# Performance work log

Hardware: AMD Instinct MI355X
Metric: run time of the kernel (lower is better)

## Reference

```python
import jax, jax.numpy as jnp
import numpy as np

B, S, H = 2, 2048, 2048
NH, NKV, HD = 16, 4, 128
NEG = -1e9


def rotate_half(x):
    x1, x2 = x[..., : x.shape[-1] // 2], x[..., x.shape[-1] // 2 :]
    return jnp.concatenate((-x2, x1), axis=-1)


def setup_inputs() -> dict:
    key = jax.random.key(0)
    ks = jax.random.split(key, 6)
    hidden_states = jax.random.normal(ks[0], (B, S, H), dtype=jnp.float32)
    # causal additive mask [B, 1, S, S]
    causal = jnp.tril(jnp.ones((S, S), dtype=bool))
    attention_mask = jnp.where(causal, 0.0, NEG).astype(jnp.float32)
    attention_mask = jnp.broadcast_to(attention_mask, (B, 1, S, S))
    # rotary embeddings, base 10000
    inv_freq = 1.0 / (10000.0 ** (np.arange(0, HD, 2, dtype=np.float32) / HD))
    pos = np.arange(S, dtype=np.float32)
    freqs = np.outer(pos, inv_freq)  # [S, HD/2]
    emb = np.concatenate([freqs, freqs], axis=-1)  # [S, HD]
    cos = jnp.broadcast_to(jnp.asarray(np.cos(emb)), (B, S, HD))
    sin = jnp.broadcast_to(jnp.asarray(np.sin(emb)), (B, S, HD))
    sc = 0.02
    Wq = jax.random.normal(ks[1], (H, NH * HD), dtype=jnp.float32) * sc
    Wk = jax.random.normal(ks[2], (H, NKV * HD), dtype=jnp.float32) * sc
    Wv = jax.random.normal(ks[3], (H, NKV * HD), dtype=jnp.float32) * sc
    Wo = jax.random.normal(ks[4], (H, H), dtype=jnp.float32) * sc
    return {"hidden_states": hidden_states, "attention_mask": attention_mask,
            "cos": cos, "sin": sin, "Wq": Wq, "Wk": Wk, "Wv": Wv, "Wo": Wo}


def reference(hidden_states, attention_mask, cos, sin, Wq, Wk, Wv, Wo):
    b, s, _ = hidden_states.shape
    # projections -> [b, heads, s, hd]
    q = (hidden_states @ Wq).reshape(b, s, NH, HD).transpose(0, 2, 1, 3)
    k = (hidden_states @ Wk).reshape(b, s, NKV, HD).transpose(0, 2, 1, 3)
    v = (hidden_states @ Wv).reshape(b, s, NKV, HD).transpose(0, 2, 1, 3)
    # RoPE (cos/sin unsqueezed at dim 1)
    c, sn = cos[:, None], sin[:, None]
    q = q * c + rotate_half(q) * sn
    k = k * c + rotate_half(k) * sn
    # GQA repeat_kv: [b, nkv, s, hd] -> [b, nh, s, hd]
    n_rep = NH // NKV
    k = jnp.repeat(k, n_rep, axis=1)
    v = jnp.repeat(v, n_rep, axis=1)
    scores = jnp.einsum("bhqd,bhkd->bhqk", q, k) / jnp.sqrt(jnp.float32(HD))
    scores = scores + attention_mask
    probs = jax.nn.softmax(scores.astype(jnp.float32), axis=-1).astype(q.dtype)
    out = jnp.einsum("bhqk,bhkd->bhqd", probs, v)
    out = out.transpose(0, 2, 1, 3).reshape(b, s, NH * HD)
    return out @ Wo
```

## Files before the change

### kernel.cpp

```cpp
#include <hip/hip_runtime.h>
#include <hip/hip_bf16.h>

typedef __bf16 bf16;
typedef __bf16 bf16x4 __attribute__((ext_vector_type(4)));
typedef __bf16 bf16x8 __attribute__((ext_vector_type(8)));
typedef float f32x4 __attribute__((ext_vector_type(4)));

__device__ __forceinline__ void gload_lds16(const void* g, void* l) {
  __builtin_amdgcn_global_load_lds((__attribute__((address_space(1))) void*)(g),
                                   (__attribute__((address_space(3))) void*)(l), 16, 0, 0);
}
__device__ __forceinline__ float fexp2(float x) {
  float r;
  asm volatile("v_exp_f32 %0, %1" : "=v"(r) : "v"(x));
  return r;
}
#define S_WAITCNT_VM(n) asm volatile("s_waitcnt vmcnt(" #n ")" ::: "memory")

__global__ void k_diag(float* __restrict__ o, float v) { o[threadIdx.x] = v; }

__global__ void k_cvt_bf16(const float* __restrict__ x, bf16* __restrict__ y, int n4) {
  int i = blockIdx.x * blockDim.x + threadIdx.x;
  if (i < n4) {
    float4 v = reinterpret_cast<const float4*>(x)[i];
    bf16x4 o = {(bf16)v.x, (bf16)v.y, (bf16)v.z, (bf16)v.w};
    reinterpret_cast<bf16x4*>(y)[i] = o;
  }
}

__global__ void k_transpose_w(const float* __restrict__ W, bf16* __restrict__ Wt, int K, int N) {
  __shared__ float tile[32][33];
  int kb = blockIdx.x * 32, nb = blockIdx.y * 32;
  int tx = threadIdx.x & 31, ty = threadIdx.x >> 5;
#pragma unroll
  for (int i = 0; i < 32; i += 8)
    tile[ty + i][tx] = W[(size_t)(kb + ty + i) * N + nb + tx];
  __syncthreads();
#pragma unroll
  for (int i = 0; i < 32; i += 8)
    Wt[(size_t)(nb + ty + i) * K + kb + tx] = (bf16)tile[tx][ty + i];
}

__global__ void k_transpose_v(const bf16* __restrict__ Cq, bf16* __restrict__ Vt) {
  __shared__ bf16 tile[32][34];
  constexpr int S = 2048, CSTR = 3072;
  int sb = blockIdx.x * 32, db = blockIdx.y * 32, bh = blockIdx.z;
  int b = bh >> 2, kvh = bh & 3;
  int tx = threadIdx.x & 31, ty = threadIdx.x >> 5;
  const bf16* src = Cq + (size_t)b * S * CSTR + 2560 + kvh * 128;
#pragma unroll
  for (int i = 0; i < 32; i += 8)
    tile[ty + i][tx] = src[(size_t)(sb + ty + i) * CSTR + db + tx];
  __syncthreads();
  bf16* dst = Vt + (size_t)bh * 128 * S;
#pragma unroll
  for (int i = 0; i < 32; i += 8)
    dst[(size_t)(db + ty + i) * S + sb + tx] = tile[tx][ty + i];
}

template <typename OT>
__global__ __launch_bounds__(512) void k_gemm3(const bf16* __restrict__ A,
                                               const bf16* __restrict__ B0,
                                               const bf16* __restrict__ B1, int nsplit,
                                               OT* __restrict__ C, int Ncols, int Kd) {
  __shared__ __align__(16) bf16 lds_[65536];
  char* lds = (char*)lds_;
  const int t = threadIdx.x, w = t >> 6, l = t & 63;
  const int lr = l & 15, lk = l >> 4;
  const int gx = gridDim.x, nwg = gx * gridDim.y;
  const int flat = blockIdx.y * gx + blockIdx.x;
  const int vid = (flat & 7) * (nwg >> 3) + (flat >> 3);
  const int m0 = (vid % gx) * 256, n0 = (vid / gx) * 256;
  const int wm = w >> 2, wn = w & 3;
  const bf16* Bt = (n0 < nsplit) ? B0 + (size_t)n0 * Kd : B1 + (size_t)(n0 - nsplit) * Kd;
  const int nkt = Kd >> 6;
  const int srow = l >> 2;
  const int lch = (l & 3) ^ ((srow + (srow >> 2)) & 3);
  auto stA = [&](int tile, int unit) {
    if (tile >= nkt) return;
    const bf16* s = A + (size_t)(m0 + unit * 64 + (w >> 1) * 16 + srow) * Kd +
                    (tile << 6) + (w & 1) * 32 + lch * 8;
    gload_lds16(s, lds + (tile & 1) * 32768 + unit * 8192 + w * 1024);
  };
  auto stB = [&](int tile, int grp) {
    if (tile >= nkt) return;
    const bf16* s = Bt + (size_t)((w >> 1) * 64 + grp * 16 + srow) * Kd +
                    (tile << 6) + (w & 1) * 32 + lch * 8;
    gload_lds16(s, lds + 65536 + (tile & 1) * 32768 + grp * 8192 + w * 1024);
  };
  const int rdoff = lr * 64 + ((lk ^ ((lr + (lr >> 2)) & 3)) << 4);

  f32x4 acc[8][4] = {};
  stA(0, 0); stA(0, 1); stA(0, 2); stA(0, 3);
  stB(0, 0);
  stA(1, 0); stB(0, 1); stA(1, 1); stB(0, 2); stA(1, 2); stB(0, 3);

  for (int kt = 0; kt < nkt; ++kt) {
    const int buf = kt & 1;
    const char* Ab = lds + buf * 32768;
    const char* Bb = lds + 65536 + buf * 32768;
    bf16x8 af[8][2];
#pragma unroll
    for (int p = 0; p < 4; ++p) {
      if (kt + 1 < nkt) { S_WAITCNT_VM(6); } else { S_WAITCNT_VM(0); }
      __builtin_amdgcn_sched_barrier(0);
      __builtin_amdgcn_s_barrier();
      __builtin_amdgcn_sched_barrier(0);
      if (p == 0) stA(kt + 1, 3); else stA(kt + 2, p - 1);
      stB(kt + 1, p);
      if (p == 0) {
#pragma unroll
        for (int i = 0; i < 8; ++i) {
          const char* ub = Ab + (wm * 2 + (i >> 2)) * 8192 + (i & 3) * 2048;
          af[i][0] = *reinterpret_cast<const bf16x8*>(ub + rdoff);
          af[i][1] = *reinterpret_cast<const bf16x8*>(ub + 1024 + rdoff);
        }
      }
      bf16x8 b0 = *reinterpret_cast<const bf16x8*>(Bb + p * 8192 + wn * 2048 + rdoff);
      bf16x8 b1 = *reinterpret_cast<const bf16x8*>(Bb + p * 8192 + wn * 2048 + 1024 + rdoff);
      __builtin_amdgcn_s_setprio(1);
#pragma unroll
      for (int i = 0; i < 8; ++i) {
        acc[i][p] = __builtin_amdgcn_mfma_f32_16x16x32_bf16(af[i][0], b0, acc[i][p], 0, 0, 0);
        acc[i][p] = __builtin_amdgcn_mfma_f32_16x16x32_bf16(af[i][1], b1, acc[i][p], 0, 0, 0);
      }
      __builtin_amdgcn_s_setprio(0);
      __builtin_amdgcn_sched_barrier(0);
    }
  }
#pragma unroll
  for (int i = 0; i < 8; ++i)
#pragma unroll
    for (int j = 0; j < 4; ++j)
#pragma unroll
      for (int r = 0; r < 4; ++r) {
        int row = m0 + wm * 128 + i * 16 + lk * 4 + r;
        int col = n0 + wn * 64 + j * 16 + lr;
        if constexpr (sizeof(OT) == 4)
          C[(size_t)row * Ncols + col] = acc[i][j][r];
        else
          C[(size_t)row * Ncols + col] = (bf16)acc[i][j][r];
      }
}

__global__ void k_rope(bf16* __restrict__ X, const float* __restrict__ cs, const float* __restrict__ sn,
                       int nh, int rowstride, float scale, int total) {
  int idx = blockIdx.x * blockDim.x + threadIdx.x;
  if (idx >= total) return;
  int d = idx & 63;
  int th = idx >> 6;
  int h = th % nh;
  int tok = th / nh;
  size_t base = (size_t)tok * rowstride + h * 128;
  float c = cs[tok * 128 + d], s = sn[tok * 128 + d];
  float x1 = (float)X[base + d];
  float x2 = (float)X[base + d + 64];
  X[base + d] = (bf16)((x1 * c - x2 * s) * scale);
  X[base + d + 64] = (bf16)((x2 * c + x1 * s) * scale);
}

__global__ __launch_bounds__(256) void k_attn(const bf16* __restrict__ Q, const bf16* __restrict__ KV,
                                              const bf16* __restrict__ Vt, bf16* __restrict__ O) {
  constexpr int S = 2048, HD = 128, QSTR = 3072, OSTR = 2048;
  __shared__ __align__(16) bf16 sK[2][64 * 128];
  __shared__ __align__(16) bf16 sV[2][128 * 64];
  __shared__ __align__(16) bf16 sP[4][16][72];
  const int bid = blockIdx.x;
  const int vid = (bid & 7) * 64 + (bid >> 3);
  const int p = vid & 15, bh = vid >> 4;
  const int h = bh & 15, b = bh >> 4;
  const int t = threadIdx.x, w = t >> 6, l = t & 63;
  const int lr = l & 15, lk = l >> 4;
  const int kvh = h >> 2;
  const int swz = (lr & 7) << 4;

  const char* kbase = (const char*)(KV + (size_t)b * S * QSTR + kvh * HD);
  const int krow_l = w * 16 + (l >> 4);
  const int kcol_l = (l & 15) << 4;
  const char* vtbase = (const char*)(Vt + (size_t)(b * 4 + kvh) * HD * S);
  const int vrow_l = w * 32 + (l >> 3);
  const int vcol_l = (l & 7) << 4;
  char* sKb = (char*)sK;
  char* sVb = (char*)sV;
  auto stage = [&](int kvb, int buf) {
#pragma unroll
    for (int c = 0; c < 4; ++c) {
      const int krow = krow_l + c * 4;
      gload_lds16(kbase + (size_t)(kvb + krow) * (QSTR * 2) + (kcol_l ^ ((krow & 7) << 4)),
                  sKb + buf * 16384 + (w * 4 + c) * 1024);
      const int vrow = vrow_l + c * 8;
      gload_lds16(vtbase + (size_t)vrow * (S * 2) + kvb * 2 + (vcol_l ^ ((vrow & 7) << 4)),
                  sVb + buf * 16384 + (w * 4 + c) * 1024);
    }
  };

  for (int seg = 0; seg < 2; ++seg) {
    const int qtl = seg ? (31 - p) : p;
    const int qw = qtl * 64 + w * 16;
    const int ntiles = qtl + 1;
    int cur = 0;
    stage(0, 0);
    const bf16* Qp = Q + (size_t)(b * S + qw + lr) * QSTR + h * HD + lk * 8;
    bf16x8 qf[4];
#pragma unroll
    for (int i = 0; i < 4; ++i) qf[i] = *reinterpret_cast<const bf16x8*>(Qp + i * 32);
    f32x4 oacc[8] = {};
    float mrow[4] = {-3e38f, -3e38f, -3e38f, -3e38f};
    float lsum[4] = {0.f, 0.f, 0.f, 0.f};
    __syncthreads();
    for (int tt = 0; tt < ntiles; ++tt) {
      const int kvb = tt * 64;
      if (tt + 1 < ntiles) stage(kvb + 64, cur ^ 1);
      const char* sKc = sKb + cur * 16384;
      const char* sVc = sVb + cur * 16384;
      float pm[4][4];
#pragma unroll
      for (int c = 0; c < 4; ++c) {
        f32x4 s4 = {};
#pragma unroll
        for (int kf = 0; kf < 4; ++kf) {
          bf16x8 kf8 = *reinterpret_cast<const bf16x8*>(
              sKc + (c * 16 + lr) * 256 + (((kf * 64) + (lk << 4)) ^ swz));
          s4 = __builtin_amdgcn_mfma_f32_16x16x32_bf16(qf[kf], kf8, s4, 0, 0, 0);
        }
#pragma unroll
        for (int r = 0; r < 4; ++r) pm[c][r] = s4[r];
      }
      if (tt == ntiles - 1) {
#pragma unroll
        for (int c = 0; c < 4; ++c) {
          const int col = kvb + c * 16 + lr;
#pragma unroll
          for (int r = 0; r < 4; ++r)
            if (col > qw + lk * 4 + r) pm[c][r] = -3e38f;
        }
      }
      float pmax[4];
#pragma unroll
      for (int r = 0; r < 4; ++r)
        pmax[r] = fmaxf(fmaxf(pm[0][r], pm[1][r]), fmaxf(pm[2][r], pm[3][r]));
      bool hi = (pmax[0] > mrow[0] + 8.f) | (pmax[1] > mrow[1] + 8.f) |
                (pmax[2] > mrow[2] + 8.f) | (pmax[3] > mrow[3] + 8.f);
      if (__any(hi)) {
        float mx[4];
#pragma unroll
        for (int r = 0; r < 4; ++r) mx[r] = pmax[r];
#pragma unroll
        for (int off = 1; off < 16; off <<= 1)
#pragma unroll
          for (int r = 0; r < 4; ++r) mx[r] = fmaxf(mx[r], __shfl_xor(mx[r], off));
#pragma unroll
        for (int r = 0; r < 4; ++r) {
          float mn = fmaxf(mrow[r], mx[r]);
          float fac = fexp2(mrow[r] - mn);
          mrow[r] = mn;
          lsum[r] *= fac;
#pragma unroll
          for (int ch = 0; ch < 8; ++ch) oacc[ch][r] *= fac;
        }
      }
#pragma unroll
      for (int c = 0; c < 4; ++c)
#pragma unroll
        for (int r = 0; r < 4; ++r) pm[c][r] = fexp2(pm[c][r] - mrow[r]);
#pragma unroll
      for (int r = 0; r < 4; ++r)
        lsum[r] += (pm[0][r] + pm[1][r]) + (pm[2][r] + pm[3][r]);
#pragma unroll
      for (int c = 0; c < 4; ++c)
#pragma unroll
        for (int r = 0; r < 4; ++r) sP[w][lk * 4 + r][c * 16 + lr] = (bf16)pm[c][r];
      bf16x8 pf0 = *reinterpret_cast<const bf16x8*>(&sP[w][lr][lk * 8]);
      bf16x8 pf1 = *reinterpret_cast<const bf16x8*>(&sP[w][lr][32 + lk * 8]);
#pragma unroll
      for (int ch = 0; ch < 8; ++ch) {
        bf16x8 vf0 = *reinterpret_cast<const bf16x8*>(
            sVc + (ch * 16 + lr) * 128 + ((lk << 4) ^ swz));
        oacc[ch] = __builtin_amdgcn_mfma_f32_16x16x32_bf16(pf0, vf0, oacc[ch], 0, 0, 0);
        bf16x8 vf1 = *reinterpret_cast<const bf16x8*>(
            sVc + (ch * 16 + lr) * 128 + ((64 + (lk << 4)) ^ swz));
        oacc[ch] = __builtin_amdgcn_mfma_f32_16x16x32_bf16(pf1, vf1, oacc[ch], 0, 0, 0);
      }
      __syncthreads();
      cur ^= 1;
    }
#pragma unroll
    for (int off = 1; off < 16; off <<= 1)
#pragma unroll
      for (int r = 0; r < 4; ++r) lsum[r] += __shfl_xor(lsum[r], off);
    float inv[4];
#pragma unroll
    for (int r = 0; r < 4; ++r) inv[r] = 1.0f / lsum[r];
    bf16* Op = O + (size_t)(b * S + qw) * OSTR + h * HD;
#pragma unroll
    for (int ch = 0; ch < 8; ++ch)
#pragma unroll
      for (int r = 0; r < 4; ++r)
        Op[(size_t)(lk * 4 + r) * OSTR + ch * 16 + lr] = (bf16)(oacc[ch][r] * inv[r]);
  }
}

extern "C" void kernel_launch(void* const* d_in, const int* in_sizes, int n_in,
                              void* d_out, int out_size, void* d_ws, size_t ws_size,
                              hipStream_t stream) {
  const float* hs = (const float*)d_in[0];
  const float* cosb = (const float*)d_in[2];
  const float* sinb = (const float*)d_in[3];
  const float* Wq = (const float*)d_in[4];
  const float* Wk = (const float*)d_in[5];
  const float* Wv = (const float*)d_in[6];
  const float* Wo = (const float*)d_in[7];
  float* out = (float*)d_out;

  constexpr int B = 2, S = 2048, H = 2048, NH = 16, NKV = 4, HD = 128;
  constexpr int T = B * S;
  constexpr size_t MB = 1024 * 1024;

  const size_t ws_need = 24 * MB;
  if (ws_size < ws_need) {
    k_diag<<<1, 64, 0, stream>>>(out, 1000.0f + (float)(ws_size / MB));
    return;
  }
  bf16* Xb = (bf16*)d_ws;
  bf16* WtQ = (bf16*)((char*)d_ws + 16 * MB);
  bf16* Ob = Xb;
  bf16* Cqkv = (bf16*)d_out;
  bf16* Vtb = (bf16*)((char*)d_out + 24 * MB);
  bf16* WtKV = (bf16*)((char*)d_out + 28 * MB);

  k_cvt_bf16<<<T * H / 4 / 256, 256, 0, stream>>>(hs, Xb, T * H / 4);

  k_transpose_w<<<dim3(H / 32, H / 32), 256, 0, stream>>>(Wq, WtQ, H, H);
  k_transpose_w<<<dim3(H / 32, (NKV * HD) / 32), 256, 0, stream>>>(Wk, WtKV, H, NKV * HD);
  k_transpose_w<<<dim3(H / 32, (NKV * HD) / 32), 256, 0, stream>>>(Wv, WtKV + (size_t)(NKV * HD) * H, H, NKV * HD);

  k_gemm3<bf16><<<dim3(16, 12), 512, 0, stream>>>(Xb, WtQ, WtKV, 2048, Cqkv, 3072, H);

  k_transpose_v<<<dim3(S / 32, HD / 32, B * NKV), 256, 0, stream>>>(Cqkv, Vtb);

  const float qscale = 0.12751743f;
  k_rope<<<(T * NH * 64) / 256, 256, 0, stream>>>(Cqkv, cosb, sinb, NH, 3072, qscale, T * NH * 64);
  k_rope<<<(T * NKV * 64) / 256, 256, 0, stream>>>(Cqkv + 2048, cosb, sinb, NKV, 3072, 1.0f, T * NKV * 64);

  k_attn<<<512, 256, 0, stream>>>(Cqkv, Cqkv + 2048, Vtb, Ob);

  k_transpose_w<<<dim3(H / 32, H / 32), 256, 0, stream>>>(Wo, WtQ, H, H);
  k_gemm3<float><<<dim3(16, 8), 512, 0, stream>>>(Ob, WtQ, WtQ, 1 << 30, out, H, H);
}
```

Before: 249.2 us.

## Restructure attention to 128-row query tiles and add 256x128 output GEMM

The attention kernel drops the two-segment load balancing and the double-buffered K/V staging. Each block now handles 128 query rows, two 16-row groups per wave, so each K/V fragment read from LDS feeds twice as many MFMAs. Staging is single-buffered with two syncthreads per tile, so loads are no longer overlapped with compute, and blocks with different causal lengths are no longer balanced. The QKV GEMM gets a new XCD-aware tile mapping, and the output projection moves to a new 256x128-tile GEMM with a two-stage prefetch pipeline and more workgroups.

```diff
diff --git a/kernel.cpp b/kernel.cpp
--- a/kernel.cpp
+++ b/kernel.cpp
@@ -67,10 +67,12 @@
   char* lds = (char*)lds_;
   const int t = threadIdx.x, w = t >> 6, l = t & 63;
   const int lr = l & 15, lk = l >> 4;
-  const int gx = gridDim.x, nwg = gx * gridDim.y;
+  const int gx = gridDim.x;
   const int flat = blockIdx.y * gx + blockIdx.x;
-  const int vid = (flat & 7) * (nwg >> 3) + (flat >> 3);
-  const int m0 = (vid % gx) * 256, n0 = (vid / gx) * 256;
+  const int xcd = flat & 7, local = flat >> 3;
+  const int mi = (xcd & 3) * (gx >> 2) + (local & ((gx >> 2) - 1));
+  const int ni = (xcd >> 2) * (gridDim.y >> 1) + (local >> 2);
+  const int m0 = mi * 256, n0 = ni * 256;
   const int wm = w >> 2, wn = w & 3;
   const bf16* Bt = (n0 < nsplit) ? B0 + (size_t)n0 * Kd : B1 + (size_t)(n0 - nsplit) * Kd;
   const int nkt = Kd >> 6;
@@ -143,6 +145,103 @@
       }
 }
 
+template <int BM, typename OT>
+__global__ __launch_bounds__(512) void k_gemm2(const bf16* __restrict__ A, const bf16* __restrict__ Bt,
+                                               OT* __restrict__ C, int N, int Kd) {
+  constexpr int NA = (BM / 16) * 2;
+  constexpr int NB = 16;
+  constexpr int NST = NA + NB;
+  constexpr int NSW = NST / 8;
+  constexpr int WM = BM / 4;
+  constexpr int RG = WM / 16;
+  __shared__ __align__(16) bf16 sAB[2][NST * 512];
+  const int t = threadIdx.x, w = t >> 6, l = t & 63;
+  const int lr = l & 15, lk = l >> 4;
+  const int gx = gridDim.x;
+  const int nwg = gx * gridDim.y;
+  const int flat = blockIdx.y * gx + blockIdx.x;
+  const int vid = (flat & 7) * (nwg >> 3) + (flat >> 3);
+  const int m0 = (vid % gx) * BM, n0 = (vid / gx) * 128;
+  const int wm = w >> 1, wn = w & 1;
+  const int srow = l >> 2;
+  const int lchunk = (l & 3) ^ (((l >> 5) & 1) << 1);
+  const int rdoff = lr * 64 + ((lk * 16) ^ ((lr >> 3) << 5));
+  const int nkt = Kd >> 6;
+  char* lds = (char*)sAB;
+
+  auto stage = [&](int kt, int buf) {
+    const int k0 = kt << 6;
+#pragma unroll
+    for (int u = 0; u < NSW; ++u) {
+      const int s = w * NSW + u;
+      const bf16* src;
+      if (s < NA)
+        src = A + (size_t)(m0 + (s >> 1) * 16 + srow) * Kd + k0 + (s & 1) * 32 + lchunk * 8;
+      else
+        src = Bt + (size_t)(n0 + ((s - NA) >> 1) * 16 + srow) * Kd + k0 + ((s - NA) & 1) * 32 + lchunk * 8;
+      gload_lds16(src, lds + buf * (NST * 1024) + s * 1024);
+    }
+  };
+
+  f32x4 acc[RG][4] = {};
+  stage(0, 0);
+  stage(1, 1);
+  if constexpr (NSW == 6) S_WAITCNT_VM(6); else S_WAITCNT_VM(4);
+  __builtin_amdgcn_s_barrier();
+  int c = 0;
+  for (int kt = 0; kt < nkt; ++kt) {
+    __builtin_amdgcn_sched_barrier(0);
+    const char* base = lds + c * (NST * 1024);
+    bf16x8 af[RG][2], bfr[4][2];
+#pragma unroll
+    for (int i = 0; i < RG; ++i)
+#pragma unroll
+      for (int kk = 0; kk < 2; ++kk)
+        af[i][kk] = *reinterpret_cast<const bf16x8*>(base + ((wm * RG + i) * 2 + kk) * 1024 + rdoff);
+#pragma unroll
+    for (int j = 0; j < 4; ++j)
+#pragma unroll
+      for (int kk = 0; kk < 2; ++kk)
+        bfr[j][kk] = *reinterpret_cast<const bf16x8*>(base + (NA + (wn * 4 + j) * 2 + kk) * 1024 + rdoff);
+    __builtin_amdgcn_s_setprio(1);
+#pragma unroll
+    for (int i = 0; i < RG; ++i)
+#pragma unroll
+      for (int j = 0; j < 4; ++j) {
+        acc[i][j] = __builtin_amdgcn_mfma_f32_16x16x32_bf16(af[i][0], bfr[j][0], acc[i][j], 0, 0, 0);
+        acc[i][j] = __builtin_amdgcn_mfma_f32_16x16x32_bf16(af[i][1], bfr[j][1], acc[i][j], 0, 0, 0);
+      }
+    __builtin_amdgcn_s_setprio(0);
+    __builtin_amdgcn_sched_barrier(0);
+    asm volatile("" ::: "memory");
+    __builtin_amdgcn_s_barrier();
+    if (kt + 2 < nkt) stage(kt + 2, c);
+    if (kt + 1 < nkt) {
+      if (kt + 2 < nkt) {
+        if constexpr (NSW == 6) S_WAITCNT_VM(6); else S_WAITCNT_VM(4);
+      } else {
+        S_WAITCNT_VM(0);
+      }
+      asm volatile("" ::: "memory");
+      __builtin_amdgcn_s_barrier();
+    }
+    c ^= 1;
+  }
+#pragma unroll
+  for (int i = 0; i < RG; ++i)
+#pragma unroll
+    for (int j = 0; j < 4; ++j)
+#pragma unroll
+      for (int r = 0; r < 4; ++r) {
+        int row = m0 + wm * WM + i * 16 + lk * 4 + r;
+        int col = n0 + wn * 64 + j * 16 + lr;
+        if constexpr (sizeof(OT) == 4)
+          C[(size_t)row * N + col] = acc[i][j][r];
+        else
+          C[(size_t)row * N + col] = (bf16)acc[i][j][r];
+      }
+}
+
 __global__ void k_rope(bf16* __restrict__ X, const float* __restrict__ cs, const float* __restrict__ sn,
                        int nh, int rowstride, float scale, int total) {
   int idx = blockIdx.x * blockDim.x + threadIdx.x;
@@ -162,12 +261,13 @@
 __global__ __launch_bounds__(256) void k_attn(const bf16* __restrict__ Q, const bf16* __restrict__ KV,
                                               const bf16* __restrict__ Vt, bf16* __restrict__ O) {
   constexpr int S = 2048, HD = 128, QSTR = 3072, OSTR = 2048;
-  __shared__ __align__(16) bf16 sK[2][64 * 128];
-  __shared__ __align__(16) bf16 sV[2][128 * 64];
-  __shared__ __align__(16) bf16 sP[4][16][72];
+  __shared__ __align__(16) bf16 sK[64 * 128];
+  __shared__ __align__(16) bf16 sV[128 * 64];
+  __shared__ __align__(16) bf16 sP[4][32][72];
   const int bid = blockIdx.x;
   const int vid = (bid & 7) * 64 + (bid >> 3);
-  const int p = vid & 15, bh = vid >> 4;
+  const int qt = 15 - (vid & 15);
+  const int bh = vid >> 4;
   const int h = bh & 15, b = bh >> 4;
   const int t = threadIdx.x, w = t >> 6, l = t & 63;
   const int lr = l & 15, lk = l >> 4;
@@ -180,123 +280,149 @@
   const char* vtbase = (const char*)(Vt + (size_t)(b * 4 + kvh) * HD * S);
   const int vrow_l = w * 32 + (l >> 3);
   const int vcol_l = (l & 7) << 4;
-  char* sKb = (char*)sK;
-  char* sVb = (char*)sV;
-  auto stage = [&](int kvb, int buf) {
+  auto stage = [&](int kvb) {
 #pragma unroll
     for (int c = 0; c < 4; ++c) {
       const int krow = krow_l + c * 4;
       gload_lds16(kbase + (size_t)(kvb + krow) * (QSTR * 2) + (kcol_l ^ ((krow & 7) << 4)),
-                  sKb + buf * 16384 + (w * 4 + c) * 1024);
+                  (char*)sK + (w * 4 + c) * 1024);
       const int vrow = vrow_l + c * 8;
       gload_lds16(vtbase + (size_t)vrow * (S * 2) + kvb * 2 + (vcol_l ^ ((vrow & 7) << 4)),
-                  sVb + buf * 16384 + (w * 4 + c) * 1024);
+                  (char*)sV + (w * 4 + c) * 1024);
     }
   };
 
-  for (int seg = 0; seg < 2; ++seg) {
-    const int qtl = seg ? (31 - p) : p;
-    const int qw = qtl * 64 + w * 16;
-    const int ntiles = qtl + 1;
-    int cur = 0;
-    stage(0, 0);
-    const bf16* Qp = Q + (size_t)(b * S + qw + lr) * QSTR + h * HD + lk * 8;
-    bf16x8 qf[4];
-#pragma unroll
-    for (int i = 0; i < 4; ++i) qf[i] = *reinterpret_cast<const bf16x8*>(Qp + i * 32);
-    f32x4 oacc[8] = {};
-    float mrow[4] = {-3e38f, -3e38f, -3e38f, -3e38f};
-    float lsum[4] = {0.f, 0.f, 0.f, 0.f};
+  const int qw = qt * 128 + w * 32;
+  const int qlast = qw + 31;
+  bf16x8 qf[2][4];
+#pragma unroll
+  for (int rg = 0; rg < 2; ++rg) {
+    const bf16* Qp = Q + (size_t)(b * S + qw + rg * 16 + lr) * QSTR + h * HD + lk * 8;
+#pragma unroll
+    for (int i = 0; i < 4; ++i) qf[rg][i] = *reinterpret_cast<const bf16x8*>(Qp + i * 32);
+  }
+  f32x4 oacc[2][8] = {};
+  float mrow[2][4] = {{-3e38f, -3e38f, -3e38f, -3e38f}, {-3e38f, -3e38f, -3e38f, -3e38f}};
+  float lsum[2][4] = {};
+  const int ntiles = (qt + 1) * 2;
+  for (int tt = 0; tt < ntiles; ++tt) {
+    const int kvb = tt * 64;
     __syncthreads();
-    for (int tt = 0; tt < ntiles; ++tt) {
-      const int kvb = tt * 64;
-      if (tt + 1 < ntiles) stage(kvb + 64, cur ^ 1);
-      const char* sKc = sKb + cur * 16384;
-      const char* sVc = sVb + cur * 16384;
-      float pm[4][4];
-#pragma unroll
-      for (int c = 0; c < 4; ++c) {
-        f32x4 s4 = {};
-#pragma unroll
-        for (int kf = 0; kf < 4; ++kf) {
-          bf16x8 kf8 = *reinterpret_cast<const bf16x8*>(
-              sKc + (c * 16 + lr) * 256 + (((kf * 64) + (lk << 4)) ^ swz));
-          s4 = __builtin_amdgcn_mfma_f32_16x16x32_bf16(qf[kf], kf8, s4, 0, 0, 0);
-        }
-#pragma unroll
-        for (int r = 0; r < 4; ++r) pm[c][r] = s4[r];
-      }
-      if (tt == ntiles - 1) {
+    stage(kvb);
+    __syncthreads();
+    if (kvb > qlast) continue;
+    float pm[2][4][4];
+#pragma unroll
+    for (int c = 0; c < 4; ++c) {
+      f32x4 s0 = {}, s1 = {};
+#pragma unroll
+      for (int kf = 0; kf < 4; ++kf) {
+        bf16x8 kf8 = *reinterpret_cast<const bf16x8*>(
+            (char*)sK + (c * 16 + lr) * 256 + (((kf * 64) + (lk << 4)) ^ swz));
+        s0 = __builtin_amdgcn_mfma_f32_16x16x32_bf16(qf[0][kf], kf8, s0, 0, 0, 0);
+        s1 = __builtin_amdgcn_mfma_f32_16x16x32_bf16(qf[1][kf], kf8, s1, 0, 0, 0);
+      }
+#pragma unroll
+      for (int r = 0; r < 4; ++r) { pm[0][c][r] = s0[r]; pm[1][c][r] = s1[r]; }
+    }
+    if (kvb + 63 > qw) {
+#pragma unroll
+      for (int rg = 0; rg < 2; ++rg)
 #pragma unroll
         for (int c = 0; c < 4; ++c) {
           const int col = kvb + c * 16 + lr;
 #pragma unroll
           for (int r = 0; r < 4; ++r)
-            if (col > qw + lk * 4 + r) pm[c][r] = -3e38f;
+            if (col > qw + rg * 16 + lk * 4 + r) pm[rg][c][r] = -3e38f;
         }
-      }
-      float pmax[4];
+    }
+    float pmax[2][4];
+#pragma unroll
+    for (int rg = 0; rg < 2; ++rg)
 #pragma unroll
       for (int r = 0; r < 4; ++r)
-        pmax[r] = fmaxf(fmaxf(pm[0][r], pm[1][r]), fmaxf(pm[2][r], pm[3][r]));
-      bool hi = (pmax[0] > mrow[0] + 8.f) | (pmax[1] > mrow[1] + 8.f) |
-                (pmax[2] > mrow[2] + 8.f) | (pmax[3] > mrow[3] + 8.f);
-      if (__any(hi)) {
-        float mx[4];
-#pragma unroll
-        for (int r = 0; r < 4; ++r) mx[r] = pmax[r];
-#pragma unroll
-        for (int off = 1; off < 16; off <<= 1)
-#pragma unroll
-          for (int r = 0; r < 4; ++r) mx[r] = fmaxf(mx[r], __shfl_xor(mx[r], off));
+        pmax[rg][r] = fmaxf(fmaxf(pm[rg][0][r], pm[rg][1][r]), fmaxf(pm[rg][2][r], pm[rg][3][r]));
+    bool hi = false;
+#pragma unroll
+    for (int rg = 0; rg < 2; ++rg)
+#pragma unroll
+      for (int r = 0; r < 4; ++r) hi |= (pmax[rg][r] > mrow[rg][r] + 8.f);
+    if (__any(hi)) {
+      float mx[2][4];
+#pragma unroll
+      for (int rg = 0; rg < 2; ++rg)
+#pragma unroll
+        for (int r = 0; r < 4; ++r) mx[rg][r] = pmax[rg][r];
+#pragma unroll
+      for (int off = 1; off < 16; off <<= 1)
+#pragma unroll
+        for (int rg = 0; rg < 2; ++rg)
+#pragma unroll
+          for (int r = 0; r < 4; ++r) mx[rg][r] = fmaxf(mx[rg][r], __shfl_xor(mx[rg][r], off));
+#pragma unroll
+      for (int rg = 0; rg < 2; ++rg)
 #pragma unroll
         for (int r = 0; r < 4; ++r) {
-          float mn = fmaxf(mrow[r], mx[r]);
-          float fac = fexp2(mrow[r] - mn);
-          mrow[r] = mn;
-          lsum[r] *= fac;
-#pragma unroll
-          for (int ch = 0; ch < 8; ++ch) oacc[ch][r] *= fac;
+          float mn = fmaxf(mrow[rg][r], mx[rg][r]);
+          float fac = fexp2(mrow[rg][r] - mn);
+          mrow[rg][r] = mn;
+          lsum[rg][r] *= fac;
+#pragma unroll
+          for (int ch = 0; ch < 8; ++ch) oacc[rg][ch][r] *= fac;
         }
-      }
+    }
+#pragma unroll
+    for (int rg = 0; rg < 2; ++rg) {
 #pragma unroll
       for (int c = 0; c < 4; ++c)
 #pragma unroll
-        for (int r = 0; r < 4; ++r) pm[c][r] = fexp2(pm[c][r] - mrow[r]);
+        for (int r = 0; r < 4; ++r) pm[rg][c][r] = fexp2(pm[rg][c][r] - mrow[rg][r]);
 #pragma unroll
       for (int r = 0; r < 4; ++r)
-        lsum[r] += (pm[0][r] + pm[1][r]) + (pm[2][r] + pm[3][r]);
+        lsum[rg][r] += (pm[rg][0][r] + pm[rg][1][r]) + (pm[rg][2][r] + pm[rg][3][r]);
+    }
+#pragma unroll
+    for (int rg = 0; rg < 2; ++rg)
 #pragma unroll
       for (int c = 0; c < 4; ++c)
 #pragma unroll
-        for (int r = 0; r < 4; ++r) sP[w][lk * 4 + r][c * 16 + lr] = (bf16)pm[c][r];
-      bf16x8 pf0 = *reinterpret_cast<const bf16x8*>(&sP[w][lr][lk * 8]);
-      bf16x8 pf1 = *reinterpret_cast<const bf16x8*>(&sP[w][lr][32 + lk * 8]);
-#pragma unroll
-      for (int ch = 0; ch < 8; ++ch) {
-        bf16x8 vf0 = *reinterpret_cast<const bf16x8*>(
-            sVc + (ch * 16 + lr) * 128 + ((lk << 4) ^ swz));
-        oacc[ch] = __builtin_amdgcn_mfma_f32_16x16x32_bf16(pf0, vf0, oacc[ch], 0, 0, 0);
-        bf16x8 vf1 = *reinterpret_cast<const bf16x8*>(
-            sVc + (ch * 16 + lr) * 128 + ((64 + (lk << 4)) ^ swz));
-        oacc[ch] = __builtin_amdgcn_mfma_f32_16x16x32_bf16(pf1, vf1, oacc[ch], 0, 0, 0);
-      }
-      __syncthreads();
-      cur ^= 1;
-    }
-#pragma unroll
-    for (int off = 1; off < 16; off <<= 1)
-#pragma unroll
-      for (int r = 0; r < 4; ++r) lsum[r] += __shfl_xor(lsum[r], off);
+        for (int r = 0; r < 4; ++r)
+          sP[w][rg * 16 + lk * 4 + r][c * 16 + lr] = (bf16)pm[rg][c][r];
+    bf16x8 pf[2][2];
+#pragma unroll
+    for (int rg = 0; rg < 2; ++rg) {
+      pf[rg][0] = *reinterpret_cast<const bf16x8*>(&sP[w][rg * 16 + lr][lk * 8]);
+      pf[rg][1] = *reinterpret_cast<const bf16x8*>(&sP[w][rg * 16 + lr][32 + lk * 8]);
+    }
+#pragma unroll
+    for (int ch = 0; ch < 8; ++ch) {
+      bf16x8 vf0 = *reinterpret_cast<const bf16x8*>(
+          (char*)sV + (ch * 16 + lr) * 128 + ((lk << 4) ^ swz));
+      bf16x8 vf1 = *reinterpret_cast<const bf16x8*>(
+          (char*)sV + (ch * 16 + lr) * 128 + ((64 + (lk << 4)) ^ swz));
+      oacc[0][ch] = __builtin_amdgcn_mfma_f32_16x16x32_bf16(pf[0][0], vf0, oacc[0][ch], 0, 0, 0);
+      oacc[0][ch] = __builtin_amdgcn_mfma_f32_16x16x32_bf16(pf[0][1], vf1, oacc[0][ch], 0, 0, 0);
+      oacc[1][ch] = __builtin_amdgcn_mfma_f32_16x16x32_bf16(pf[1][0], vf0, oacc[1][ch], 0, 0, 0);
+      oacc[1][ch] = __builtin_amdgcn_mfma_f32_16x16x32_bf16(pf[1][1], vf1, oacc[1][ch], 0, 0, 0);
+    }
+  }
+#pragma unroll
+  for (int off = 1; off < 16; off <<= 1)
+#pragma unroll
+    for (int rg = 0; rg < 2; ++rg)
+#pragma unroll
+      for (int r = 0; r < 4; ++r) lsum[rg][r] += __shfl_xor(lsum[rg][r], off);
+#pragma unroll
+  for (int rg = 0; rg < 2; ++rg) {
     float inv[4];
 #pragma unroll
-    for (int r = 0; r < 4; ++r) inv[r] = 1.0f / lsum[r];
-    bf16* Op = O + (size_t)(b * S + qw) * OSTR + h * HD;
+    for (int r = 0; r < 4; ++r) inv[r] = 1.0f / lsum[rg][r];
+    bf16* Op = O + (size_t)(b * S + qw + rg * 16) * OSTR + h * HD;
 #pragma unroll
     for (int ch = 0; ch < 8; ++ch)
 #pragma unroll
       for (int r = 0; r < 4; ++r)
-        Op[(size_t)(lk * 4 + r) * OSTR + ch * 16 + lr] = (bf16)(oacc[ch][r] * inv[r]);
+        Op[(size_t)(lk * 4 + r) * OSTR + ch * 16 + lr] = (bf16)(oacc[rg][ch][r] * inv[r]);
   }
 }
 
@@ -345,5 +471,5 @@
   k_attn<<<512, 256, 0, stream>>>(Cqkv, Cqkv + 2048, Vtb, Ob);
 
   k_transpose_w<<<dim3(H / 32, H / 32), 256, 0, stream>>>(Wo, WtQ, H, H);
-  k_gemm3<float><<<dim3(16, 8), 512, 0, stream>>>(Ob, WtQ, WtQ, 1 << 30, out, H, H);
-}
+  k_gemm2<256, float><<<dim3(16, 16), 512, 0, stream>>>(Ob, WtQ, out, H, H);
+}
```

Measured after the change: 271.7 us. 1.09x slower.
